# Kernel tuning notes

Measured on AMD Instinct MI355X. Metric: run time of the kernel, lower is better.

The kernel has to match this reference:

```python
import jax, jax.numpy as jnp
import numpy as np

V = 25          # skeleton joints (NTU)
C = 128         # channels (input == output)
FRAMES = 300    # frames per sequence
B = 8           # sequences
T = B * FRAMES  # total frames = 2400
K = 4           # temporal half-window (kernel=9 -> +-4)
EPS = 1e-5


def _temporal_edges():
    # +-1..K frame neighbors within each FRAMES-long block, plus self loops.
    t = np.arange(T)
    blk = t // FRAMES
    src, dst = [], []
    for d in range(1, K + 1):
        for s in (d, -d):
            d_idx = t + s
            valid = (d_idx >= 0) & (d_idx < T) & (blk == np.clip(d_idx, 0, T - 1) // FRAMES)
            src.append(t[valid]); dst.append(d_idx[valid])
    src.append(t); dst.append(t)  # self loops (utils.add_self_loops)
    return np.concatenate(src).astype(np.int32), np.concatenate(dst).astype(np.int32)


def setup_inputs() -> dict:
    key = jax.random.key(0)
    ks = jax.random.split(key, 6)
    x = jax.random.normal(ks[0], (T, V, C), dtype=jnp.float32)
    # 3-partition skeleton adjacency (dense [3,25,25], sparse-ish)
    A = jax.random.uniform(ks[1], (3, V, V), dtype=jnp.float32)
    A = A * (jax.random.uniform(ks[2], (3, V, V)) < 0.25).astype(jnp.float32)
    edge_importance = jnp.ones((3, V, V), dtype=jnp.float32)
    Ws = jax.random.normal(ks[3], (3, C, C), dtype=jnp.float32) * 0.05
    bs = jnp.zeros((3, C), dtype=jnp.float32)
    Wt = jax.random.normal(ks[4], (C, C), dtype=jnp.float32) * 0.05
    bt = jnp.zeros((C,), dtype=jnp.float32)
    gamma = jnp.ones((V * C,), dtype=jnp.float32)
    beta = jnp.zeros((V * C,), dtype=jnp.float32)
    src, dst = _temporal_edges()
    edge_index = jnp.asarray(np.stack([src, dst]))  # [2, E]
    edge_weight = jnp.ones((edge_index.shape[1],), dtype=jnp.float32)
    return {"x": x, "A": A, "edge_importance": edge_importance, "Ws": Ws,
            "bs": bs, "Wt": Wt, "bt": bt, "gamma": gamma, "beta": beta,
            "edge_weight": edge_weight, "edge_index": edge_index}


def _group_norm(h, gamma, beta):
    # Norm('gn', C*25): single-group normalization over (V*C) per frame, affine.
    f = h.reshape(h.shape[0], -1)
    mu = jnp.mean(f, axis=-1, keepdims=True)
    var = jnp.var(f, axis=-1, keepdims=True)
    f = (f - mu) * jax.lax.rsqrt(var + EPS) * gamma + beta
    return f.reshape(h.shape)


def reference(x, A, edge_importance, Ws, bs, Wt, bt, gamma, beta, edge_weight, edge_index):
    # --- Net_nodes: 3 spatial GCN branches with cached dense adj, summed ---
    Aeff = A * edge_importance                       # [3,V,V]
    xw = jnp.einsum('tvc,icd->itvd', x, Ws)          # per-branch x @ W_i
    h = jnp.einsum('iuv,itvd->tud', Aeff, xw) + jnp.sum(bs, axis=0)  # [T,V,C]
    # --- gn + relu ---
    h = jax.nn.relu(_group_norm(h, gamma, beta))
    # --- temporal GCNConv (normalize=False) over frame graph ---
    xW = jnp.einsum('tvc,cd->tvd', h, Wt)            # [T,V,C]
    src, dst = edge_index[0], edge_index[1]
    msgs = xW[src] * edge_weight[:, None, None]      # [E,V,C]
    agg = jax.ops.segment_sum(msgs, dst, num_segments=T) + bt
    # residual=False path: data_final.x = x (temporal conv out) + 0, then relu.
    # (Second gn + dropout output is overwritten by `data_final['x'] = x`.)
    return jax.nn.relu(agg)
```

## Files before the change

### kernel.cpp

```cpp
#include <hip/hip_runtime.h>

#define T_FRAMES 2400
#define V 25
#define C 128
#define VC 3200
#define NB 3
#define GN_EPS 1e-5f
#define MAXDEG 16
#define KS 384
#define K2 96
#define CSTR 136
#define KSTR 104
#define AGG_STRIDE 136
#define FPB 4
#define WMAX 48

typedef __attribute__((ext_vector_type(8))) short short8;
typedef __attribute__((ext_vector_type(4))) float floatx4;
typedef unsigned short u16;
typedef unsigned int u32;

__device__ __forceinline__ u16 f2bf(float f) {
    u32 u = __builtin_bit_cast(u32, f);
    u += 0x7FFFu + ((u >> 16) & 1u);
    return (u16)(u >> 16);
}
__device__ __forceinline__ float bf2f(u16 h) {
    u32 u = ((u32)h) << 16;
    return __builtin_bit_cast(float, u);
}

__global__ __launch_bounds__(256) void k_prep(
        const float* __restrict__ Ws, const float* __restrict__ Wt,
        const float* __restrict__ A, const float* __restrict__ EI,
        const float* __restrict__ bs,
        u16* __restrict__ Wsw, u16* __restrict__ Wtsw, u16* __restrict__ Msw,
        float* __restrict__ bsum, int* __restrict__ deg)
{
    const int idx = blockIdx.x * 256 + threadIdx.x;
    if (idx < KS * C) {
        const int j = idx & 7, n = (idx >> 3) & 127, kg = idx >> 10;
        const int k = kg * 8 + j;
        Wsw[idx] = f2bf(Ws[k * C + n]);
    }
    if (idx < C * C) {
        const int j = idx & 7, n = (idx >> 3) & 127, kg = idx >> 10;
        const int k = kg * 8 + j;
        Wtsw[idx] = f2bf(Wt[k * C + n]);
    }
    if (idx < 32 * K2) {
        const int u = idx / K2, r = idx % K2;
        const int i = r >> 5, v = r & 31;
        float val = 0.f;
        if (u < V && v < V) {
            const int a = (i * V + u) * V + v;
            val = A[a] * EI[a];
        }
        Msw[idx] = f2bf(val);
    }
    if (idx < C) bsum[idx] = bs[idx] + bs[C + idx] + bs[2 * C + idx];
    if (idx < T_FRAMES) deg[idx] = 0;
}

__global__ __launch_bounds__(256) void k_scatter(
        const int* __restrict__ eidx, const float* __restrict__ ew, int E,
        int* __restrict__ deg, int* __restrict__ adjsrc, float* __restrict__ adjw) {
    const int e = blockIdx.x * 256 + threadIdx.x;
    if (e >= E) return;
    const int s = eidx[e];
    const int d = eidx[E + e];
    const int slot = atomicAdd(&deg[d], 1);
    if (slot < MAXDEG) {
        adjsrc[d * MAXDEG + slot] = s;
        adjw  [d * MAXDEG + slot] = ew[e];
    }
}

__global__ __launch_bounds__(512) void k_spatial(
        const float* __restrict__ x, const u16* __restrict__ Wsw,
        const u16* __restrict__ Msw, const float* __restrict__ bsum_g,
        const float* __restrict__ gamma_g, const float* __restrict__ beta_g,
        u16* __restrict__ h_g)
{
    __shared__ u16 xt[32 * CSTR];
    __shared__ u16 yb[C * KSTR];
    __shared__ float redS[8], redQ[8];

    const int tid = threadIdx.x;
    const int w   = tid >> 6;
    const int l   = tid & 63;
    const int q   = l >> 4;
    const int ln  = l & 15;
    const int col = w * 16 + ln;
    const int t   = blockIdx.x;

    for (int i = tid; i < 7 * CSTR; i += 512) xt[25 * CSTR + i] = 0;

    const float bsv = bsum_g[col];

    if (tid < 400) {
        const int srow = tid >> 4;
        const int sc0  = (tid & 15) * 8;
        const float* xp = x + (size_t)t * VC + srow * C + sc0;
        const float4 v0 = *(const float4*)xp;
        const float4 v1 = *(const float4*)(xp + 4);
        u32 pk[4];
        pk[0] = (u32)f2bf(v0.x) | ((u32)f2bf(v0.y) << 16);
        pk[1] = (u32)f2bf(v0.z) | ((u32)f2bf(v0.w) << 16);
        pk[2] = (u32)f2bf(v1.x) | ((u32)f2bf(v1.y) << 16);
        pk[3] = (u32)f2bf(v1.z) | ((u32)f2bf(v1.w) << 16);
        *reinterpret_cast<uint4*>(&xt[srow * CSTR + sc0]) = *reinterpret_cast<uint4*>(pk);
    }
    __syncthreads();

    #pragma unroll 1
    for (int i = 0; i < 3; i++) {
        short8 wfr[4];
        #pragma unroll
        for (int s = 0; s < 4; s++)
            wfr[s] = *reinterpret_cast<const short8*>(
                Wsw + (((i * 4 + s) * 4 + q) * C + col) * 8);
        floatx4 ta = {0,0,0,0}, tb = {0,0,0,0};
        #pragma unroll
        for (int s = 0; s < 4; s++) {
            const short8 bx0 = *reinterpret_cast<const short8*>(&xt[ln * CSTR + s * 32 + q * 8]);
            const short8 bx1 = *reinterpret_cast<const short8*>(&xt[(16 + ln) * CSTR + s * 32 + q * 8]);
            ta = __builtin_amdgcn_mfma_f32_16x16x32_bf16(wfr[s], bx0, ta, 0, 0, 0);
            tb = __builtin_amdgcn_mfma_f32_16x16x32_bf16(wfr[s], bx1, tb, 0, 0, 0);
        }
        #pragma unroll
        for (int r = 0; r < 4; r++) {
            const int d = w * 16 + q * 4 + r;
            yb[d * KSTR + i * 32 + ln]      = f2bf(ta[r]);
            yb[d * KSTR + i * 32 + 16 + ln] = f2bf(tb[r]);
        }
    }
    __syncthreads();

    floatx4 h0 = {0,0,0,0}, h1 = {0,0,0,0};
    {
        short8 mfr[2][3];
        #pragma unroll
        for (int tile = 0; tile < 2; tile++)
            #pragma unroll
            for (int i2 = 0; i2 < 3; i2++)
                mfr[tile][i2] = *reinterpret_cast<const short8*>(
                    Msw + (tile * 16 + ln) * K2 + i2 * 32 + q * 8);
        #pragma unroll
        for (int i2 = 0; i2 < 3; i2++) {
            const short8 b2 = *reinterpret_cast<const short8*>(&yb[col * KSTR + i2 * 32 + q * 8]);
            h0 = __builtin_amdgcn_mfma_f32_16x16x32_bf16(mfr[0][i2], b2, h0, 0, 0, 0);
            h1 = __builtin_amdgcn_mfma_f32_16x16x32_bf16(mfr[1][i2], b2, h1, 0, 0, 0);
        }
    }

    float s_p = 0.f, q_p = 0.f;
    #pragma unroll
    for (int r = 0; r < 4; r++) {
        h0[r] += bsv;
        s_p += h0[r]; q_p = fmaf(h0[r], h0[r], q_p);
    }
    #pragma unroll
    for (int r = 0; r < 4; r++) {
        h1[r] += bsv;
        if (q * 4 + r < 9) { s_p += h1[r]; q_p = fmaf(h1[r], h1[r], q_p); }
    }
    #pragma unroll
    for (int off = 32; off; off >>= 1) {
        s_p += __shfl_down(s_p, off);
        q_p += __shfl_down(q_p, off);
    }
    if (l == 0) { redS[w] = s_p; redQ[w] = q_p; }
    __syncthreads();

    float S = 0.f, Q = 0.f;
    #pragma unroll
    for (int i = 0; i < 8; i++) { S += redS[i]; Q += redQ[i]; }
    const float mu  = S / (float)VC;
    const float var = Q / (float)VC - mu * mu;
    const float rs  = rsqrtf(fmaxf(var, 0.f) + GN_EPS);

    u16* hp = h_g + (size_t)t * VC;
    #pragma unroll
    for (int r = 0; r < 4; r++) {
        const int idx = (q * 4 + r) * C + col;
        const float v = (h0[r] - mu) * rs * gamma_g[idx] + beta_g[idx];
        hp[idx] = f2bf(v > 0.f ? v : 0.f);
    }
    #pragma unroll
    for (int r = 0; r < 4; r++) {
        const int row = 16 + q * 4 + r;
        if (row < V) {
            const int idx = row * C + col;
            const float v = (h1[r] - mu) * rs * gamma_g[idx] + beta_g[idx];
            hp[idx] = f2bf(v > 0.f ? v : 0.f);
        }
    }
}

__global__ __launch_bounds__(512) void k_temporal(
        const u16* __restrict__ h, const int* __restrict__ deg,
        const int* __restrict__ adjsrc, const float* __restrict__ adjw,
        const u16* __restrict__ Wtsw, const float* __restrict__ bt,
        float* __restrict__ out)
{
    __shared__ u16   agg[FPB * 32 * AGG_STRIDE];
    __shared__ float wmat[FPB][WMAX];
    __shared__ int   s_src[FPB * MAXDEG];
    __shared__ float s_wv[FPB * MAXDEG];
    __shared__ int   s_deg[FPB];
    __shared__ int   s_info[2];

    const int tid = threadIdx.x;
    const int w   = tid >> 6;
    const int l   = tid & 63;
    const int q   = l >> 4;
    const int ln  = l & 15;
    const int col = w * 16 + ln;
    const int t0  = blockIdx.x * FPB;

    if (tid < FPB * MAXDEG) {
        const int tf = tid >> 4;
        s_src[tid] = adjsrc[(t0 + tf) * MAXDEG + (tid & 15)];
        s_wv[tid]  = adjw  [(t0 + tf) * MAXDEG + (tid & 15)];
    }
    if (tid >= 64 && tid < 64 + FPB) s_deg[tid - 64] = min(deg[t0 + tid - 64], MAXDEG);
    if (tid >= 128 && tid < 128 + FPB * WMAX) wmat[(tid - 128) / WMAX][(tid - 128) % WMAX] = 0.f;
    for (int i = tid; i < FPB * 7 * AGG_STRIDE; i += 512) {
        const int fr = i / (7 * AGG_STRIDE), rem = i % (7 * AGG_STRIDE);
        agg[fr * 32 * AGG_STRIDE + 25 * AGG_STRIDE + rem] = 0;
    }
    __syncthreads();

    if (tid < 64) {
        const int fe = tid >> 4, e = tid & 15;
        const bool valid = e < s_deg[fe];
        int sv = valid ? s_src[tid] : 0x7fffffff;
        int sx = valid ? s_src[tid] : (int)0x80000000;
        #pragma unroll
        for (int off = 32; off; off >>= 1) {
            sv = min(sv, __shfl_down(sv, off));
            sx = max(sx, __shfl_down(sx, off));
        }
        if (tid == 0) {
            s_info[0] = sv;
            s_info[1] = (sx >= sv) ? (sx - sv + 1) : 0;
        }
    }
    __syncthreads();
    const int minS = s_info[0];
    const int nsrc = s_info[1];
    const bool windowed = (nsrc > 0) && (nsrc <= WMAX);
    if (windowed && tid < 64) {
        const int fe = tid >> 4, e = tid & 15;
        if (e < s_deg[fe]) atomicAdd(&wmat[fe][s_src[tid] - minS], s_wv[tid]);
    }
    __syncthreads();

    if (tid < V * 16) {
        const int row = tid >> 4;
        const int c8  = (tid & 15) * 8;
        float a0[8] = {0,0,0,0,0,0,0,0}, a1[8] = {0,0,0,0,0,0,0,0};
        float a2[8] = {0,0,0,0,0,0,0,0}, a3[8] = {0,0,0,0,0,0,0,0};
        if (windowed) {
            const u16* hb = h + (size_t)minS * VC + row * C + c8;
            for (int s = 0; s < nsrc; s++) {
                const short8 hv = *reinterpret_cast<const short8*>(hb + (size_t)s * VC);
                const float w0 = wmat[0][s], w1 = wmat[1][s];
                const float w2 = wmat[2][s], w3 = wmat[3][s];
                #pragma unroll
                for (int j = 0; j < 8; j++) {
                    const float xv = bf2f((u16)hv[j]);
                    a0[j] = fmaf(w0, xv, a0[j]);
                    a1[j] = fmaf(w1, xv, a1[j]);
                    a2[j] = fmaf(w2, xv, a2[j]);
                    a3[j] = fmaf(w3, xv, a3[j]);
                }
            }
        } else {
            #pragma unroll
            for (int fe = 0; fe < FPB; fe++) {
                float* af = fe == 0 ? a0 : fe == 1 ? a1 : fe == 2 ? a2 : a3;
                for (int e = 0; e < s_deg[fe]; e++) {
                    const short8 hv = *reinterpret_cast<const short8*>(
                        h + (size_t)s_src[fe * MAXDEG + e] * VC + row * C + c8);
                    const float wv = s_wv[fe * MAXDEG + e];
                    #pragma unroll
                    for (int j = 0; j < 8; j++) af[j] = fmaf(wv, bf2f((u16)hv[j]), af[j]);
                }
            }
        }
        const float* accs[4] = {a0, a1, a2, a3};
        #pragma unroll
        for (int fe = 0; fe < FPB; fe++) {
            u32 pk[4];
            #pragma unroll
            for (int i = 0; i < 4; i++)
                pk[i] = (u32)f2bf(accs[fe][2 * i]) | ((u32)f2bf(accs[fe][2 * i + 1]) << 16);
            *reinterpret_cast<uint4*>(&agg[(fe * 32 + row) * AGG_STRIDE + c8]) =
                *reinterpret_cast<uint4*>(pk);
        }
    }
    __syncthreads();

    short8 bfr[4];
    #pragma unroll
    for (int s = 0; s < 4; s++)
        bfr[s] = *reinterpret_cast<const short8*>(Wtsw + ((s * 4 + q) * C + col) * 8);
    const float btv = bt[col];

    #pragma unroll 1
    for (int fe = 0; fe < FPB; fe++) {
        floatx4 acc0 = {0,0,0,0}, acc1 = {0,0,0,0};
        const u16* ab = &agg[fe * 32 * AGG_STRIDE];
        #pragma unroll
        for (int s = 0; s < 4; s++) {
            const short8 a0 = *reinterpret_cast<const short8*>(&ab[ln * AGG_STRIDE + s * 32 + q * 8]);
            const short8 a1 = *reinterpret_cast<const short8*>(&ab[(16 + ln) * AGG_STRIDE + s * 32 + q * 8]);
            acc0 = __builtin_amdgcn_mfma_f32_16x16x32_bf16(a0, bfr[s], acc0, 0, 0, 0);
            acc1 = __builtin_amdgcn_mfma_f32_16x16x32_bf16(a1, bfr[s], acc1, 0, 0, 0);
        }
        float* op = out + (size_t)(t0 + fe) * VC;
        #pragma unroll
        for (int r = 0; r < 4; r++) {
            const float v = acc0[r] + btv;
            op[(q * 4 + r) * C + col] = v > 0.f ? v : 0.f;
        }
        #pragma unroll
        for (int r = 0; r < 4; r++) {
            const int row = 16 + q * 4 + r;
            if (row < V) {
                const float v = acc1[r] + btv;
                op[row * C + col] = v > 0.f ? v : 0.f;
            }
        }
    }
}

extern "C" void kernel_launch(void* const* d_in, const int* in_sizes, int n_in,
                              void* d_out, int out_size, void* d_ws, size_t ws_size,
                              hipStream_t stream) {
    const float* x     = (const float*)d_in[0];
    const float* A     = (const float*)d_in[1];
    const float* EI    = (const float*)d_in[2];
    const float* Ws    = (const float*)d_in[3];
    const float* bs    = (const float*)d_in[4];
    const float* Wt    = (const float*)d_in[5];
    const float* bt    = (const float*)d_in[6];
    const float* gamma = (const float*)d_in[7];
    const float* beta  = (const float*)d_in[8];
    const float* ew    = (const float*)d_in[9];
    const int*   eidx  = (const int*)d_in[10];
    const int E = in_sizes[9];

    char* ws = (char*)d_ws;
    u16*   h      = (u16*)(ws);
    u16*   Wsw    = (u16*)(ws + 15360000);
    u16*   Wtsw   = (u16*)(ws + 15458304);
    u16*   Msw    = (u16*)(ws + 15491072);
    float* bsum   = (float*)(ws + 15497216);
    int*   deg    = (int*)(ws + 15497728);
    int*   adjsrc = (int*)(ws + 15507328);
    float* adjw   = (float*)(ws + 15660928);

    float* out = (float*)d_out;

    k_prep<<<(KS * C + 255) / 256, 256, 0, stream>>>(Ws, Wt, A, EI, bs, Wsw, Wtsw, Msw, bsum, deg);
    k_scatter<<<(E + 255) / 256, 256, 0, stream>>>(eidx, ew, E, deg, adjsrc, adjw);
    k_spatial<<<T_FRAMES, 512, 0, stream>>>(x, Wsw, Msw, bsum, gamma, beta, h);
    k_temporal<<<T_FRAMES / FPB, 512, 0, stream>>>(h, deg, adjsrc, adjw, Wtsw, bt, out);
}
```

Baseline: 138.4 us.

## Process one frame per block in temporal kernel instead of four

Measured after the change: 151.2 us. 1.09x slower.

```diff
diff --git a/kernel.cpp b/kernel.cpp
--- a/kernel.cpp
+++ b/kernel.cpp
@@ -12,8 +12,7 @@
 #define CSTR 136
 #define KSTR 104
 #define AGG_STRIDE 136
-#define FPB 4
-#define WMAX 48
+#define WMAX 32
 
 typedef __attribute__((ext_vector_type(8))) short short8;
 typedef __attribute__((ext_vector_type(4))) float floatx4;
@@ -204,12 +203,11 @@
         const u16* __restrict__ Wtsw, const float* __restrict__ bt,
         float* __restrict__ out)
 {
-    __shared__ u16   agg[FPB * 32 * AGG_STRIDE];
-    __shared__ float wmat[FPB][WMAX];
-    __shared__ int   s_src[FPB * MAXDEG];
-    __shared__ float s_wv[FPB * MAXDEG];
-    __shared__ int   s_deg[FPB];
-    __shared__ int   s_info[2];
+    __shared__ u16   agg[32 * AGG_STRIDE];
+    __shared__ float wvec[WMAX];
+    __shared__ int   s_src[MAXDEG];
+    __shared__ float s_wv[MAXDEG];
+    __shared__ int   s_info[3];
 
     const int tid = threadIdx.x;
     const int w   = tid >> 6;
@@ -217,89 +215,66 @@
     const int q   = l >> 4;
     const int ln  = l & 15;
     const int col = w * 16 + ln;
-    const int t0  = blockIdx.x * FPB;
-
-    if (tid < FPB * MAXDEG) {
-        const int tf = tid >> 4;
-        s_src[tid] = adjsrc[(t0 + tf) * MAXDEG + (tid & 15)];
-        s_wv[tid]  = adjw  [(t0 + tf) * MAXDEG + (tid & 15)];
-    }
-    if (tid >= 64 && tid < 64 + FPB) s_deg[tid - 64] = min(deg[t0 + tid - 64], MAXDEG);
-    if (tid >= 128 && tid < 128 + FPB * WMAX) wmat[(tid - 128) / WMAX][(tid - 128) % WMAX] = 0.f;
-    for (int i = tid; i < FPB * 7 * AGG_STRIDE; i += 512) {
-        const int fr = i / (7 * AGG_STRIDE), rem = i % (7 * AGG_STRIDE);
-        agg[fr * 32 * AGG_STRIDE + 25 * AGG_STRIDE + rem] = 0;
-    }
-    __syncthreads();
-
-    if (tid < 64) {
-        const int fe = tid >> 4, e = tid & 15;
-        const bool valid = e < s_deg[fe];
+    const int t   = blockIdx.x;
+
+    if (tid < MAXDEG) {
+        s_src[tid] = adjsrc[t * MAXDEG + tid];
+        s_wv[tid]  = adjw  [t * MAXDEG + tid];
+    }
+    if (tid == MAXDEG) s_info[0] = min(deg[t], MAXDEG);
+    if (tid >= 32 && tid < 32 + WMAX) wvec[tid - 32] = 0.f;
+    for (int i = tid; i < 7 * AGG_STRIDE; i += 512) agg[25 * AGG_STRIDE + i] = 0;
+    __syncthreads();
+
+    const int dg = s_info[0];
+    if (tid < 16) {
+        const bool valid = tid < dg;
         int sv = valid ? s_src[tid] : 0x7fffffff;
         int sx = valid ? s_src[tid] : (int)0x80000000;
         #pragma unroll
-        for (int off = 32; off; off >>= 1) {
+        for (int off = 8; off; off >>= 1) {
             sv = min(sv, __shfl_down(sv, off));
             sx = max(sx, __shfl_down(sx, off));
         }
         if (tid == 0) {
-            s_info[0] = sv;
-            s_info[1] = (sx >= sv) ? (sx - sv + 1) : 0;
-        }
-    }
-    __syncthreads();
-    const int minS = s_info[0];
-    const int nsrc = s_info[1];
+            s_info[1] = sv;
+            s_info[2] = (sx >= sv) ? (sx - sv + 1) : 0;
+        }
+    }
+    __syncthreads();
+    const int minS = s_info[1];
+    const int nsrc = s_info[2];
     const bool windowed = (nsrc > 0) && (nsrc <= WMAX);
-    if (windowed && tid < 64) {
-        const int fe = tid >> 4, e = tid & 15;
-        if (e < s_deg[fe]) atomicAdd(&wmat[fe][s_src[tid] - minS], s_wv[tid]);
-    }
+    if (windowed && tid < dg) atomicAdd(&wvec[s_src[tid] - minS], s_wv[tid]);
     __syncthreads();
 
     if (tid < V * 16) {
         const int row = tid >> 4;
         const int c8  = (tid & 15) * 8;
-        float a0[8] = {0,0,0,0,0,0,0,0}, a1[8] = {0,0,0,0,0,0,0,0};
-        float a2[8] = {0,0,0,0,0,0,0,0}, a3[8] = {0,0,0,0,0,0,0,0};
+        float a0[8] = {0,0,0,0,0,0,0,0};
         if (windowed) {
             const u16* hb = h + (size_t)minS * VC + row * C + c8;
             for (int s = 0; s < nsrc; s++) {
                 const short8 hv = *reinterpret_cast<const short8*>(hb + (size_t)s * VC);
-                const float w0 = wmat[0][s], w1 = wmat[1][s];
-                const float w2 = wmat[2][s], w3 = wmat[3][s];
+                const float wv = wvec[s];
                 #pragma unroll
-                for (int j = 0; j < 8; j++) {
-                    const float xv = bf2f((u16)hv[j]);
-                    a0[j] = fmaf(w0, xv, a0[j]);
-                    a1[j] = fmaf(w1, xv, a1[j]);
-                    a2[j] = fmaf(w2, xv, a2[j]);
-                    a3[j] = fmaf(w3, xv, a3[j]);
-                }
+                for (int j = 0; j < 8; j++) a0[j] = fmaf(wv, bf2f((u16)hv[j]), a0[j]);
             }
         } else {
-            #pragma unroll
-            for (int fe = 0; fe < FPB; fe++) {
-                float* af = fe == 0 ? a0 : fe == 1 ? a1 : fe == 2 ? a2 : a3;
-                for (int e = 0; e < s_deg[fe]; e++) {
-                    const short8 hv = *reinterpret_cast<const short8*>(
-                        h + (size_t)s_src[fe * MAXDEG + e] * VC + row * C + c8);
-                    const float wv = s_wv[fe * MAXDEG + e];
-                    #pragma unroll
-                    for (int j = 0; j < 8; j++) af[j] = fmaf(wv, bf2f((u16)hv[j]), af[j]);
-                }
+            for (int e = 0; e < dg; e++) {
+                const short8 hv = *reinterpret_cast<const short8*>(
+                    h + (size_t)s_src[e] * VC + row * C + c8);
+                const float wv = s_wv[e];
+                #pragma unroll
+                for (int j = 0; j < 8; j++) a0[j] = fmaf(wv, bf2f((u16)hv[j]), a0[j]);
             }
         }
-        const float* accs[4] = {a0, a1, a2, a3};
-        #pragma unroll
-        for (int fe = 0; fe < FPB; fe++) {
-            u32 pk[4];
-            #pragma unroll
-            for (int i = 0; i < 4; i++)
-                pk[i] = (u32)f2bf(accs[fe][2 * i]) | ((u32)f2bf(accs[fe][2 * i + 1]) << 16);
-            *reinterpret_cast<uint4*>(&agg[(fe * 32 + row) * AGG_STRIDE + c8]) =
-                *reinterpret_cast<uint4*>(pk);
-        }
+        u32 pk[4];
+        #pragma unroll
+        for (int i = 0; i < 4; i++)
+            pk[i] = (u32)f2bf(a0[2 * i]) | ((u32)f2bf(a0[2 * i + 1]) << 16);
+        *reinterpret_cast<uint4*>(&agg[row * AGG_STRIDE + c8]) =
+            *reinterpret_cast<uint4*>(pk);
     }
     __syncthreads();
 
@@ -309,30 +284,26 @@
         bfr[s] = *reinterpret_cast<const short8*>(Wtsw + ((s * 4 + q) * C + col) * 8);
     const float btv = bt[col];
 
-    #pragma unroll 1
-    for (int fe = 0; fe < FPB; fe++) {
-        floatx4 acc0 = {0,0,0,0}, acc1 = {0,0,0,0};
-        const u16* ab = &agg[fe * 32 * AGG_STRIDE];
-        #pragma unroll
-        for (int s = 0; s < 4; s++) {
-            const short8 a0 = *reinterpret_cast<const short8*>(&ab[ln * AGG_STRIDE + s * 32 + q * 8]);
-            const short8 a1 = *reinterpret_cast<const short8*>(&ab[(16 + ln) * AGG_STRIDE + s * 32 + q * 8]);
-            acc0 = __builtin_amdgcn_mfma_f32_16x16x32_bf16(a0, bfr[s], acc0, 0, 0, 0);
-            acc1 = __builtin_amdgcn_mfma_f32_16x16x32_bf16(a1, bfr[s], acc1, 0, 0, 0);
-        }
-        float* op = out + (size_t)(t0 + fe) * VC;
-        #pragma unroll
-        for (int r = 0; r < 4; r++) {
-            const float v = acc0[r] + btv;
-            op[(q * 4 + r) * C + col] = v > 0.f ? v : 0.f;
-        }
-        #pragma unroll
-        for (int r = 0; r < 4; r++) {
-            const int row = 16 + q * 4 + r;
-            if (row < V) {
-                const float v = acc1[r] + btv;
-                op[row * C + col] = v > 0.f ? v : 0.f;
-            }
+    floatx4 acc0 = {0,0,0,0}, acc1 = {0,0,0,0};
+    #pragma unroll
+    for (int s = 0; s < 4; s++) {
+        const short8 a0 = *reinterpret_cast<const short8*>(&agg[ln * AGG_STRIDE + s * 32 + q * 8]);
+        const short8 a1 = *reinterpret_cast<const short8*>(&agg[(16 + ln) * AGG_STRIDE + s * 32 + q * 8]);
+        acc0 = __builtin_amdgcn_mfma_f32_16x16x32_bf16(a0, bfr[s], acc0, 0, 0, 0);
+        acc1 = __builtin_amdgcn_mfma_f32_16x16x32_bf16(a1, bfr[s], acc1, 0, 0, 0);
+    }
+    float* op = out + (size_t)t * VC;
+    #pragma unroll
+    for (int r = 0; r < 4; r++) {
+        const float v = acc0[r] + btv;
+        op[(q * 4 + r) * C + col] = v > 0.f ? v : 0.f;
+    }
+    #pragma unroll
+    for (int r = 0; r < 4; r++) {
+        const int row = 16 + q * 4 + r;
+        if (row < V) {
+            const float v = acc1[r] + btv;
+            op[row * C + col] = v > 0.f ? v : 0.f;
         }
     }
 }
@@ -368,5 +339,5 @@
     k_prep<<<(KS * C + 255) / 256, 256, 0, stream>>>(Ws, Wt, A, EI, bs, Wsw, Wtsw, Msw, bsum, deg);
     k_scatter<<<(E + 255) / 256, 256, 0, stream>>>(eidx, ew, E, deg, adjsrc, adjw);
     k_spatial<<<T_FRAMES, 512, 0, stream>>>(x, Wsw, Msw, bsum, gamma, beta, h);
-    k_temporal<<<T_FRAMES / FPB, 512, 0, stream>>>(h, deg, adjsrc, adjw, Wtsw, bt, out);
-}
+    k_temporal<<<T_FRAMES, 512, 0, stream>>>(h, deg, adjsrc, adjw, Wtsw, bt, out);
+}
```
